# Performance work log

Hardware: AMD Instinct MI355X
Metric: run time of the kernel (lower is better)

Reference implementation:

```python
import jax, jax.numpy as jnp
import numpy as np
import math

N_NODES = 50000
N_EDGES = 640000
IN_FEATS = 128
HEADS = 8
OUT_FEATS = 16
D_FF = 4 * IN_FEATS


def setup_inputs() -> dict:
    key = jax.random.key(0)
    ks = jax.random.split(key, 10)
    s = 0.05
    return {
        "feat": jax.random.normal(ks[0], (N_NODES, IN_FEATS), jnp.float32),
        "src": jax.random.randint(ks[1], (N_EDGES,), 0, N_NODES, jnp.int32),
        "dst": jax.random.randint(ks[2], (N_EDGES,), 0, N_NODES, jnp.int32),
        "Wq": jax.random.normal(ks[3], (IN_FEATS, HEADS * OUT_FEATS), jnp.float32) * s,
        "Wk": jax.random.normal(ks[4], (IN_FEATS, HEADS * OUT_FEATS), jnp.float32) * s,
        "Wv": jax.random.normal(ks[5], (IN_FEATS, HEADS * OUT_FEATS), jnp.float32) * s,
        "ln1_g": jnp.ones((IN_FEATS,), jnp.float32),
        "ln1_b": jnp.zeros((IN_FEATS,), jnp.float32),
        "W1": jax.random.normal(ks[6], (IN_FEATS, D_FF), jnp.float32) * s,
        "b1": jnp.zeros((D_FF,), jnp.float32),
        "prelu_a": jnp.full((D_FF,), 0.25, jnp.float32),  # torch PReLU default init
        "W2": jax.random.normal(ks[7], (D_FF, IN_FEATS), jnp.float32) * s,
        "b2": jnp.zeros((IN_FEATS,), jnp.float32),
    }


def layer_norm(x, g, b, eps=1e-5):
    mu = jnp.mean(x, axis=-1, keepdims=True)
    var = jnp.mean(jnp.square(x - mu), axis=-1, keepdims=True)
    return (x - mu) * jax.lax.rsqrt(var + eps) * g + b


def reference(feat, src, dst, Wq, Wk, Wv, ln1_g, ln1_b, W1, b1, prelu_a, W2, b2):
    N = feat.shape[0]
    feat_c = jax.lax.stop_gradient(feat)  # feat.clone().detach()
    q = (feat @ Wq).reshape(N, HEADS, OUT_FEATS)
    k = (feat_c @ Wk).reshape(N, HEADS, OUT_FEATS)
    v = (feat_c @ Wv).reshape(N, HEADS, OUT_FEATS)

    # edge score: dot(k[src], q[dst]) per head -> [E, H]
    e = jnp.einsum('ehd,ehd->eh', k[src], q[dst]) / math.sqrt(OUT_FEATS * HEADS)

    # segment softmax over incoming edges of each dst node
    m = jax.ops.segment_max(e, dst, num_segments=N)          # [N, H]
    e_exp = jnp.exp(e - m[dst])                              # [E, H]
    denom = jax.ops.segment_sum(e_exp, dst, num_segments=N)  # [N, H]
    a = e_exp / denom[dst]                                   # [E, H]

    # weighted scatter-sum aggregation
    msg = v[src] * a[:, :, None]                             # [E, H, D]
    ft2 = jax.ops.segment_sum(msg, dst, num_segments=N)      # [N, H, D]

    rst = ft2.reshape(feat.shape) + feat
    # NOTE: original applies ln1 twice (ln2 is unused) -- reproduced faithfully
    rst = layer_norm(rst, ln1_g, ln1_b)
    h = rst @ W1 + b1
    h = jnp.where(h >= 0, h, prelu_a * h)                    # PReLU, per-channel
    ffn = h @ W2 + b2
    rst = layer_norm(rst + ffn, ln1_g, ln1_b)
    return rst
```

## Files before the change

kernel.cpp:

```cpp
#include <hip/hip_runtime.h>

#define N_NODES 50000
#define N_EDGES 640000
#define F 128
#define DFF 512
#define NB 196

using u32 = unsigned int;
using u16 = unsigned short;

typedef __bf16 bf16x8 __attribute__((ext_vector_type(8)));
typedef float f32x4 __attribute__((ext_vector_type(4)));

__device__ __forceinline__ float bf2f(u16 u) {
    return __uint_as_float(((u32)u) << 16);
}
__device__ __forceinline__ float blo(u32 p) { return __uint_as_float(p << 16); }
__device__ __forceinline__ float bhi(u32 p) { return __uint_as_float(p & 0xffff0000u); }
__device__ __forceinline__ u16 f2bf(float f) {
    u32 u = __float_as_uint(f);
    u += 0x7fffu + ((u >> 16) & 1u);
    return (u16)(u >> 16);
}
__device__ __forceinline__ u32 pack2(float a, float b) {
    return (u32)f2bf(a) | ((u32)f2bf(b) << 16);
}

__global__ void k_hist(const int* __restrict__ dst, int* __restrict__ cnt) {
    int e = blockIdx.x * 256 + threadIdx.x;
    if (e < N_EDGES) atomicAdd(&cnt[dst[e]], 1);
}

__global__ void k_bsum(const int* __restrict__ counts, int* __restrict__ bsum) {
    int i = blockIdx.x * 256 + threadIdx.x;
    int v = (i < N_NODES) ? counts[i] : 0;
#pragma unroll
    for (int off = 32; off >= 1; off >>= 1) v += __shfl_xor(v, off, 64);
    __shared__ int ws[4];
    int lane = threadIdx.x & 63, wid = threadIdx.x >> 6;
    if (lane == 0) ws[wid] = v;
    __syncthreads();
    if (threadIdx.x == 0) bsum[blockIdx.x] = ws[0] + ws[1] + ws[2] + ws[3];
}

__global__ void k_bscan(const int* __restrict__ bsum, int* __restrict__ boff) {
    int t = threadIdx.x;
    int v = (t < NB) ? bsum[t] : 0;
    int lane = t & 63, wid = t >> 6;
    int incl = v;
#pragma unroll
    for (int off = 1; off < 64; off <<= 1) {
        int u = __shfl_up(incl, off, 64);
        if (lane >= off) incl += u;
    }
    __shared__ int ws[4];
    if (lane == 63) ws[wid] = incl;
    __syncthreads();
    int wo = 0;
#pragma unroll
    for (int j = 0; j < 4; ++j) if (j < wid) wo += ws[j];
    if (t < NB) boff[t] = wo + incl - v;
}

__global__ void k_bfill(const int* __restrict__ counts, const int* __restrict__ boff,
                        int* __restrict__ row_ptr) {
    int b = blockIdx.x, t = threadIdx.x;
    int i = b * 256 + t;
    int v = (i < N_NODES) ? counts[i] : 0;
    int lane = t & 63, wid = t >> 6;
    int incl = v;
#pragma unroll
    for (int off = 1; off < 64; off <<= 1) {
        int u = __shfl_up(incl, off, 64);
        if (lane >= off) incl += u;
    }
    __shared__ int ws[4];
    if (lane == 63) ws[wid] = incl;
    __syncthreads();
    int wo = 0;
#pragma unroll
    for (int j = 0; j < 4; ++j) if (j < wid) wo += ws[j];
    if (i < N_NODES) row_ptr[i] = boff[b] + wo + incl - v;
    if (i == 0) row_ptr[N_NODES] = N_EDGES;
}

__global__ void k_fill(const int* __restrict__ src, const int* __restrict__ dst,
                       const int* __restrict__ row_ptr, int* __restrict__ fill,
                       int* __restrict__ csr_src) {
    int e = blockIdx.x * 256 + threadIdx.x;
    if (e < N_EDGES) {
        int d = dst[e];
        int pos = row_ptr[d] + atomicAdd(&fill[d], 1);
        csr_src[pos] = src[e];
    }
}

#define FEAT_UNITS (N_NODES * F / 4)
__global__ void k_prep(const float* __restrict__ feat, u16* __restrict__ featb,
                       const float* __restrict__ Wq, const float* __restrict__ Wk,
                       const float* __restrict__ Wv, const float* __restrict__ W1,
                       const float* __restrict__ W2, u16* __restrict__ WT) {
    int idx = blockIdx.x * 256 + threadIdx.x;
    if (idx < FEAT_UNITS) {
        float4 v = reinterpret_cast<const float4*>(feat)[idx];
        uint2 p;
        p.x = pack2(v.x, v.y);
        p.y = pack2(v.z, v.w);
        reinterpret_cast<uint2*>(featb)[idx] = p;
        return;
    }
    int wi = idx - FEAT_UNITS;
    if (wi >= 180224) return;
    if (wi < 49152) {
        int mi = wi >> 14;
        int local = wi & 16383;
        const float* W = (mi == 0) ? Wq : ((mi == 1) ? Wk : Wv);
        int n = local >> 7, k = local & 127;
        WT[wi] = f2bf(W[(size_t)k * 128 + n]);
    } else if (wi < 114688) {
        int local = wi - 49152;
        int n = local >> 7, k = local & 127;
        WT[wi] = f2bf(W1[(size_t)k * 512 + n]);
    } else {
        int local = wi - 114688;
        int n = local >> 9, k = local & 511;
        WT[wi] = f2bf(W2[(size_t)k * 128 + n]);
    }
}

template <int EPI>
__global__ __launch_bounds__(256) void k_mm(
    const u16* __restrict__ A, int lda,
    const u16* __restrict__ BT,
    void* __restrict__ Cv, int ldc,
    int K,
    const float* __restrict__ bias,
    const float* __restrict__ prelu,
    const u16* __restrict__ resid,
    const float* __restrict__ g,
    const float* __restrict__ bb)
{
    __shared__ u16 smem[17408];
    u16* sA = smem;
    u16* sB = smem + 128 * 64;
    u16* sC = smem;

    const int t = threadIdx.x;
    const int w = t >> 6;
    const int lane = t & 63;
    const int ln = lane & 15, q4 = lane >> 4;
    const int row0 = blockIdx.x * 128;
    const int cb = blockIdx.y * 128;

    f32x4 acc[2][8];
#pragma unroll
    for (int mt = 0; mt < 2; ++mt)
#pragma unroll
        for (int nt = 0; nt < 8; ++nt)
            acc[mt][nt] = (f32x4){0.f, 0.f, 0.f, 0.f};

    uint4 pa[4], pb[4];
#define LOAD_A(kc)                                                             \
    {                                                                          \
        _Pragma("unroll") for (int i = 0; i < 4; ++i) {                        \
            int u = i * 256 + t, r = u >> 3, k8 = (u & 7) * 8;                 \
            int row = row0 + r;                                                \
            uint4 val = make_uint4(0, 0, 0, 0);                                \
            if (row < N_NODES)                                                 \
                val = *reinterpret_cast<const uint4*>(A + (size_t)row * lda + (kc) + k8); \
            pa[i] = val;                                                       \
        }                                                                      \
    }
#define LOAD_B(kc)                                                             \
    {                                                                          \
        _Pragma("unroll") for (int i = 0; i < 4; ++i) {                        \
            int u = i * 256 + t, r = u >> 3, k8 = (u & 7) * 8;                 \
            pb[i] = *reinterpret_cast<const uint4*>(BT + (size_t)(cb + r) * K + (kc) + k8); \
        }                                                                      \
    }

    LOAD_A(0);
    LOAD_B(0);

    for (int kc = 0; kc < K; kc += 64) {
#pragma unroll
        for (int i = 0; i < 4; ++i) {
            int u = i * 256 + t, r = u >> 3, gi = u & 7;
            int off = (r * 8 + (gi ^ (r & 7))) * 8;
            *reinterpret_cast<uint4*>(&sA[off]) = pa[i];
            *reinterpret_cast<uint4*>(&sB[off]) = pb[i];
        }
        __syncthreads();
        if (kc + 64 < K) {
            LOAD_A(kc + 64);
            LOAD_B(kc + 64);
        }
#pragma unroll
        for (int ks = 0; ks < 2; ++ks) {
            const int gsw = ks * 4 + q4;
            const int rA0 = w * 32 + ln;
            const int rA1 = rA0 + 16;
            bf16x8 a0 = *reinterpret_cast<const bf16x8*>(&sA[(rA0 * 8 + (gsw ^ (rA0 & 7))) * 8]);
            bf16x8 a1 = *reinterpret_cast<const bf16x8*>(&sA[(rA1 * 8 + (gsw ^ (rA1 & 7))) * 8]);
#pragma unroll
            for (int nt = 0; nt < 8; ++nt) {
                const int rB = nt * 16 + ln;
                bf16x8 b = *reinterpret_cast<const bf16x8*>(&sB[(rB * 8 + (gsw ^ (rB & 7))) * 8]);
                acc[0][nt] = __builtin_amdgcn_mfma_f32_16x16x32_bf16(a0, b, acc[0][nt], 0, 0, 0);
                acc[1][nt] = __builtin_amdgcn_mfma_f32_16x16x32_bf16(a1, b, acc[1][nt], 0, 0, 0);
            }
        }
        __syncthreads();
    }
#undef LOAD_A
#undef LOAD_B

    if (EPI == 0 || EPI == 1) {
        float bs[8], pr[8];
        if (EPI == 1) {
#pragma unroll
            for (int nt = 0; nt < 8; ++nt) {
                int col = cb + nt * 16 + ln;
                bs[nt] = bias[col];
                pr[nt] = prelu[col];
            }
        }
#pragma unroll
        for (int mt = 0; mt < 2; ++mt)
#pragma unroll
            for (int nt = 0; nt < 8; ++nt)
#pragma unroll
                for (int j = 0; j < 4; ++j) {
                    float x = acc[mt][nt][j];
                    if (EPI == 1) {
                        x += bs[nt];
                        x = (x >= 0.f) ? x : pr[nt] * x;
                    }
                    sC[(w * 32 + mt * 16 + q4 * 4 + j) * 136 + nt * 16 + ln] = f2bf(x);
                }
        __syncthreads();
        if (EPI == 0 && cb != 0) {
            u32* C32 = (u32*)Cv;
            const u32 vflag = (cb == 256) ? 1u : 0u;
#pragma unroll
            for (int i = 0; i < 8; ++i) {
                int u = i * 256 + t;
                int r = u >> 4, c8 = (u & 15) * 8;
                int row = row0 + r;
                if (row < N_NODES) {
                    const u32* srow = reinterpret_cast<const u32*>(&sC[r * 136 + c8]);
                    u32 dw = (u32)row * 192u + 64u + (u32)c8 + vflag;
                    C32[dw]     = srow[0];
                    C32[dw + 2] = srow[1];
                    C32[dw + 4] = srow[2];
                    C32[dw + 6] = srow[3];
                }
            }
        } else {
            u16* C = (u16*)Cv;
#pragma unroll
            for (int i = 0; i < 8; ++i) {
                int u = i * 256 + t;
                int r = u >> 4, c8 = (u & 15) * 8;
                int row = row0 + r;
                if (row < N_NODES) {
                    uint4 val = *reinterpret_cast<const uint4*>(&sC[r * 136 + c8]);
                    *reinterpret_cast<uint4*>(&C[(size_t)row * ldc + cb + c8]) = val;
                }
            }
        }
    } else {
        float* C = (float*)Cv;
        float bs[8], gv[8], bv[8];
#pragma unroll
        for (int nt = 0; nt < 8; ++nt) {
            int col = nt * 16 + ln;
            bs[nt] = bias[col];
            gv[nt] = g[col];
            bv[nt] = bb[col];
        }
#pragma unroll
        for (int mt = 0; mt < 2; ++mt)
#pragma unroll
            for (int j = 0; j < 4; ++j) {
                int row = row0 + w * 32 + mt * 16 + q4 * 4 + j;
                bool ok = row < N_NODES;
                float vals[8];
                float s = 0.f, ss = 0.f;
#pragma unroll
                for (int nt = 0; nt < 8; ++nt) {
                    float x = acc[mt][nt][j] + bs[nt];
                    if (ok) x += bf2f(resid[(size_t)row * 128 + nt * 16 + ln]);
                    vals[nt] = x;
                    s += x; ss += x * x;
                }
                s += __shfl_xor(s, 8, 16); ss += __shfl_xor(ss, 8, 16);
                s += __shfl_xor(s, 4, 16); ss += __shfl_xor(ss, 4, 16);
                s += __shfl_xor(s, 2, 16); ss += __shfl_xor(ss, 2, 16);
                s += __shfl_xor(s, 1, 16); ss += __shfl_xor(ss, 1, 16);
                float mu = s * (1.f / 128.f);
                float var = ss * (1.f / 128.f) - mu * mu;
                float rs = rsqrtf(var + 1e-5f);
                if (ok) {
#pragma unroll
                    for (int nt = 0; nt < 8; ++nt)
                        C[(size_t)row * 128 + nt * 16 + ln] =
                            (vals[nt] - mu) * rs * gv[nt] + bv[nt];
                }
            }
    }
}

__global__ __launch_bounds__(256) void k_attn(
    const u32* __restrict__ Q32, const float* __restrict__ feat,
    const int* __restrict__ row_ptr, const int* __restrict__ csr_src,
    const float* __restrict__ g, const float* __restrict__ bb,
    u16* __restrict__ rstb)
{
    const int w = threadIdx.x >> 6;
    const int lane = threadIdx.x & 63;
    const int n = blockIdx.x * 4 + w;
    if (n >= N_NODES) return;
    const float scale = 0.08838834764831845f;

    const u32 qp = Q32[(u32)n * 192u + (u32)lane];
    const float q0 = blo(qp), q1 = bhi(qp);
    const int e0 = row_ptr[n], e1 = row_ptr[n + 1];
    const u32 kvlane = 64u + 2u * (u32)lane;

    float l = 0.f, a0 = 0.f, a1 = 0.f;

#define LD4(S, KV)                                                                      \
    {                                                                                   \
        KV[0] = *reinterpret_cast<const uint2*>(Q32 + (u32)(S).x * 192u + kvlane);      \
        KV[1] = *reinterpret_cast<const uint2*>(Q32 + (u32)(S).y * 192u + kvlane);      \
        KV[2] = *reinterpret_cast<const uint2*>(Q32 + (u32)(S).z * 192u + kvlane);      \
        KV[3] = *reinterpret_cast<const uint2*>(Q32 + (u32)(S).w * 192u + kvlane);      \
    }
#define CG(KV)                                                                          \
    {                                                                                   \
        float p0 = blo(KV[0].x) * q0 + bhi(KV[0].x) * q1;                               \
        float p1 = blo(KV[1].x) * q0 + bhi(KV[1].x) * q1;                               \
        float p2 = blo(KV[2].x) * q0 + bhi(KV[2].x) * q1;                               \
        float p3 = blo(KV[3].x) * q0 + bhi(KV[3].x) * q1;                               \
        p0 += __shfl_xor(p0, 4, 8); p1 += __shfl_xor(p1, 4, 8);                         \
        p2 += __shfl_xor(p2, 4, 8); p3 += __shfl_xor(p3, 4, 8);                         \
        p0 += __shfl_xor(p0, 2, 8); p1 += __shfl_xor(p1, 2, 8);                         \
        p2 += __shfl_xor(p2, 2, 8); p3 += __shfl_xor(p3, 2, 8);                         \
        p0 += __shfl_xor(p0, 1, 8); p1 += __shfl_xor(p1, 1, 8);                         \
        p2 += __shfl_xor(p2, 1, 8); p3 += __shfl_xor(p3, 1, 8);                         \
        float ea = __expf(p0 * scale), eb = __expf(p1 * scale);                         \
        float ec = __expf(p2 * scale), ed = __expf(p3 * scale);                         \
        l += (ea + eb) + (ec + ed);                                                     \
        a0 += ea * blo(KV[0].y) + eb * blo(KV[1].y) + ec * blo(KV[2].y) + ed * blo(KV[3].y); \
        a1 += ea * bhi(KV[0].y) + eb * bhi(KV[1].y) + ec * bhi(KV[2].y) + ed * bhi(KV[3].y); \
    }

    const int rem = e1 - e0;
    const int ng = rem >> 2;
    {
        int4 sA, sB, sCc;
        uint2 kvA[4], kvB[4], kvC[4];
        if (ng >= 1) { sA = *reinterpret_cast<const int4*>(csr_src + e0);      LD4(sA, kvA); }
        if (ng >= 2) { sB = *reinterpret_cast<const int4*>(csr_src + e0 + 4);  LD4(sB, kvB); }
        if (ng >= 3) { sCc = *reinterpret_cast<const int4*>(csr_src + e0 + 8); LD4(sCc, kvC); }
        int gq = 0;
        while (gq + 6 <= ng) {
            CG(kvA); sA = *reinterpret_cast<const int4*>(csr_src + e0 + (gq + 3) * 4); LD4(sA, kvA);
            CG(kvB); sB = *reinterpret_cast<const int4*>(csr_src + e0 + (gq + 4) * 4); LD4(sB, kvB);
            CG(kvC); sCc = *reinterpret_cast<const int4*>(csr_src + e0 + (gq + 5) * 4); LD4(sCc, kvC);
            gq += 3;
        }
        const int r = ng - gq;
        if (r == 1) { CG(kvA); }
        else if (r == 2) { CG(kvA); CG(kvB); }
        else if (r == 3) { CG(kvA); CG(kvB); CG(kvC); }
        else if (r == 4) {
            CG(kvA); sA = *reinterpret_cast<const int4*>(csr_src + e0 + (gq + 3) * 4); LD4(sA, kvA);
            CG(kvB); CG(kvC); CG(kvA);
        } else if (r == 5) {
            CG(kvA); sA = *reinterpret_cast<const int4*>(csr_src + e0 + (gq + 3) * 4); LD4(sA, kvA);
            CG(kvB); sB = *reinterpret_cast<const int4*>(csr_src + e0 + (gq + 4) * 4); LD4(sB, kvB);
            CG(kvC); CG(kvA); CG(kvB);
        }
    }
    for (int e = e0 + ng * 4; e < e1; ++e) {
        int s0 = csr_src[e];
        uint2 kv = *reinterpret_cast<const uint2*>(Q32 + (u32)s0 * 192u + kvlane);
        float p0 = blo(kv.x) * q0 + bhi(kv.x) * q1;
        p0 += __shfl_xor(p0, 4, 8);
        p0 += __shfl_xor(p0, 2, 8);
        p0 += __shfl_xor(p0, 1, 8);
        float ea = __expf(p0 * scale);
        l += ea;
        a0 += ea * blo(kv.y);
        a1 += ea * bhi(kv.y);
    }
#undef LD4
#undef CG

    float inv = (l > 0.f) ? 1.f / l : 0.f;
    const int c2 = lane * 2;
    const float2 fr = *reinterpret_cast<const float2*>(feat + (size_t)n * 128 + c2);
    float x0 = a0 * inv + fr.x;
    float x1 = a1 * inv + fr.y;

    float sum = x0 + x1, sq = x0 * x0 + x1 * x1;
#pragma unroll
    for (int off = 32; off >= 1; off >>= 1) {
        sum += __shfl_xor(sum, off, 64);
        sq += __shfl_xor(sq, off, 64);
    }
    float mu = sum * (1.f / 128.f);
    float var = sq * (1.f / 128.f) - mu * mu;
    float rs = rsqrtf(var + 1e-5f);
    float y0 = (x0 - mu) * rs * g[c2] + bb[c2];
    float y1 = (x1 - mu) * rs * g[c2 + 1] + bb[c2 + 1];
    reinterpret_cast<u32*>(rstb)[(size_t)n * 64 + lane] = pack2(y0, y1);
}

extern "C" void kernel_launch(void* const* d_in, const int* in_sizes, int n_in,
                              void* d_out, int out_size, void* d_ws, size_t ws_size,
                              hipStream_t stream)
{
    const float* feat = (const float*)d_in[0];
    const int* src    = (const int*)d_in[1];
    const int* dst    = (const int*)d_in[2];
    const float* Wq   = (const float*)d_in[3];
    const float* Wk   = (const float*)d_in[4];
    const float* Wv   = (const float*)d_in[5];
    const float* ln_g = (const float*)d_in[6];
    const float* ln_b = (const float*)d_in[7];
    const float* W1   = (const float*)d_in[8];
    const float* b1   = (const float*)d_in[9];
    const float* pa   = (const float*)d_in[10];
    const float* W2   = (const float*)d_in[11];
    const float* b2   = (const float*)d_in[12];

    u16* qkv   = (u16*)d_ws;
    u16* h     = qkv + (size_t)N_NODES * 384;
    u16* featb = h;
    u16* rstb  = h + (size_t)N_NODES * 512;
    u16* WT    = rstb + (size_t)N_NODES * 128;
    u16* BqkvT = WT;
    u16* W1T   = WT + 49152;
    u16* W2T   = WT + 114688;
    int* counts  = (int*)(WT + 180224);
    int* fill    = counts + N_NODES;
    int* row_ptr = fill + N_NODES;
    int* csr_src = row_ptr + N_NODES + 1;
    int* bsum    = csr_src + N_EDGES;
    int* boff    = bsum + NB;

    k_prep<<<(FEAT_UNITS + 180224 + 255) / 256, 256, 0, stream>>>(
        feat, featb, Wq, Wk, Wv, W1, W2, WT);

    hipMemsetAsync(counts, 0, sizeof(int) * 2 * N_NODES, stream);
    k_hist<<<(N_EDGES + 255) / 256, 256, 0, stream>>>(dst, counts);
    k_bsum<<<NB, 256, 0, stream>>>(counts, bsum);
    k_bscan<<<1, 256, 0, stream>>>(bsum, boff);
    k_bfill<<<NB, 256, 0, stream>>>(counts, boff, row_ptr);
    k_fill<<<(N_EDGES + 255) / 256, 256, 0, stream>>>(src, dst, row_ptr, fill, csr_src);

    const int MBK = (N_NODES + 127) / 128;

    dim3 gqkv(MBK, 3);
    k_mm<0><<<gqkv, 256, 0, stream>>>(featb, 128, BqkvT, qkv, 384, 128,
                                      nullptr, nullptr, nullptr, nullptr, nullptr);

    k_attn<<<(N_NODES + 3) / 4, 256, 0, stream>>>((const u32*)qkv, feat, row_ptr, csr_src,
                                                  ln_g, ln_b, rstb);

    dim3 gf1(MBK, 4);
    k_mm<1><<<gf1, 256, 0, stream>>>(rstb, 128, W1T, h, 512, 128,
                                     b1, pa, nullptr, nullptr, nullptr);

    dim3 gf2(MBK, 1);
    k_mm<2><<<gf2, 256, 0, stream>>>(h, 512, W2T, d_out, 128, 512,
                                     b2, nullptr, rstb, ln_g, ln_b);
}
```

Measured before the change: 350.9 us.

## Fuse histogram into prep, merge block scan into fill, simplify attention prefetch

```diff
diff --git a/kernel.cpp b/kernel.cpp
--- a/kernel.cpp
+++ b/kernel.cpp
@@ -26,8 +26,42 @@
     return (u32)f2bf(a) | ((u32)f2bf(b) << 16);
 }
 
-__global__ void k_hist(const int* __restrict__ dst, int* __restrict__ cnt) {
-    int e = blockIdx.x * 256 + threadIdx.x;
+#define FEAT_UNITS (N_NODES * F / 4)
+#define PH_TOTAL (FEAT_UNITS + 180224 + N_EDGES)
+__global__ void k_prep(const float* __restrict__ feat, u16* __restrict__ featb,
+                       const float* __restrict__ Wq, const float* __restrict__ Wk,
+                       const float* __restrict__ Wv, const float* __restrict__ W1,
+                       const float* __restrict__ W2, u16* __restrict__ WT,
+                       const int* __restrict__ dst, int* __restrict__ cnt) {
+    int idx = blockIdx.x * 256 + threadIdx.x;
+    if (idx < FEAT_UNITS) {
+        float4 v = reinterpret_cast<const float4*>(feat)[idx];
+        uint2 p;
+        p.x = pack2(v.x, v.y);
+        p.y = pack2(v.z, v.w);
+        reinterpret_cast<uint2*>(featb)[idx] = p;
+        return;
+    }
+    int wi = idx - FEAT_UNITS;
+    if (wi < 180224) {
+        if (wi < 49152) {
+            int mi = wi >> 14;
+            int local = wi & 16383;
+            const float* W = (mi == 0) ? Wq : ((mi == 1) ? Wk : Wv);
+            int n = local >> 7, k = local & 127;
+            WT[wi] = f2bf(W[(size_t)k * 128 + n]);
+        } else if (wi < 114688) {
+            int local = wi - 49152;
+            int n = local >> 7, k = local & 127;
+            WT[wi] = f2bf(W1[(size_t)k * 512 + n]);
+        } else {
+            int local = wi - 114688;
+            int n = local >> 9, k = local & 511;
+            WT[wi] = f2bf(W2[(size_t)k * 128 + n]);
+        }
+        return;
+    }
+    int e = wi - 180224;
     if (e < N_EDGES) atomicAdd(&cnt[dst[e]], 1);
 }
 
@@ -43,44 +77,43 @@
     if (threadIdx.x == 0) bsum[blockIdx.x] = ws[0] + ws[1] + ws[2] + ws[3];
 }
 
-__global__ void k_bscan(const int* __restrict__ bsum, int* __restrict__ boff) {
-    int t = threadIdx.x;
-    int v = (t < NB) ? bsum[t] : 0;
+__global__ void k_bfill(const int* __restrict__ counts, const int* __restrict__ bsum,
+                        int* __restrict__ row_ptr) {
+    int b = blockIdx.x, t = threadIdx.x;
     int lane = t & 63, wid = t >> 6;
+    __shared__ int ws[4];
+    __shared__ int sboff[256];
+
+    int bv = (t < NB) ? bsum[t] : 0;
+    int bincl = bv;
+#pragma unroll
+    for (int off = 1; off < 64; off <<= 1) {
+        int u = __shfl_up(bincl, off, 64);
+        if (lane >= off) bincl += u;
+    }
+    if (lane == 63) ws[wid] = bincl;
+    __syncthreads();
+    int bwo = 0;
+#pragma unroll
+    for (int j = 0; j < 4; ++j) if (j < wid) bwo += ws[j];
+    sboff[t] = bwo + bincl - bv;
+    __syncthreads();
+    const int boff = sboff[b];
+
+    int i = b * 256 + t;
+    int v = (i < N_NODES) ? counts[i] : 0;
     int incl = v;
 #pragma unroll
     for (int off = 1; off < 64; off <<= 1) {
         int u = __shfl_up(incl, off, 64);
         if (lane >= off) incl += u;
     }
-    __shared__ int ws[4];
     if (lane == 63) ws[wid] = incl;
     __syncthreads();
     int wo = 0;
 #pragma unroll
     for (int j = 0; j < 4; ++j) if (j < wid) wo += ws[j];
-    if (t < NB) boff[t] = wo + incl - v;
-}
-
-__global__ void k_bfill(const int* __restrict__ counts, const int* __restrict__ boff,
-                        int* __restrict__ row_ptr) {
-    int b = blockIdx.x, t = threadIdx.x;
-    int i = b * 256 + t;
-    int v = (i < N_NODES) ? counts[i] : 0;
-    int lane = t & 63, wid = t >> 6;
-    int incl = v;
-#pragma unroll
-    for (int off = 1; off < 64; off <<= 1) {
-        int u = __shfl_up(incl, off, 64);
-        if (lane >= off) incl += u;
-    }
-    __shared__ int ws[4];
-    if (lane == 63) ws[wid] = incl;
-    __syncthreads();
-    int wo = 0;
-#pragma unroll
-    for (int j = 0; j < 4; ++j) if (j < wid) wo += ws[j];
-    if (i < N_NODES) row_ptr[i] = boff[b] + wo + incl - v;
+    if (i < N_NODES) row_ptr[i] = boff + wo + incl - v;
     if (i == 0) row_ptr[N_NODES] = N_EDGES;
 }
 
@@ -92,39 +125,6 @@
         int d = dst[e];
         int pos = row_ptr[d] + atomicAdd(&fill[d], 1);
         csr_src[pos] = src[e];
-    }
-}
-
-#define FEAT_UNITS (N_NODES * F / 4)
-__global__ void k_prep(const float* __restrict__ feat, u16* __restrict__ featb,
-                       const float* __restrict__ Wq, const float* __restrict__ Wk,
-                       const float* __restrict__ Wv, const float* __restrict__ W1,
-                       const float* __restrict__ W2, u16* __restrict__ WT) {
-    int idx = blockIdx.x * 256 + threadIdx.x;
-    if (idx < FEAT_UNITS) {
-        float4 v = reinterpret_cast<const float4*>(feat)[idx];
-        uint2 p;
-        p.x = pack2(v.x, v.y);
-        p.y = pack2(v.z, v.w);
-        reinterpret_cast<uint2*>(featb)[idx] = p;
-        return;
-    }
-    int wi = idx - FEAT_UNITS;
-    if (wi >= 180224) return;
-    if (wi < 49152) {
-        int mi = wi >> 14;
-        int local = wi & 16383;
-        const float* W = (mi == 0) ? Wq : ((mi == 1) ? Wk : Wv);
-        int n = local >> 7, k = local & 127;
-        WT[wi] = f2bf(W[(size_t)k * 128 + n]);
-    } else if (wi < 114688) {
-        int local = wi - 49152;
-        int n = local >> 7, k = local & 127;
-        WT[wi] = f2bf(W1[(size_t)k * 512 + n]);
-    } else {
-        int local = wi - 114688;
-        int n = local >> 9, k = local & 511;
-        WT[wi] = f2bf(W2[(size_t)k * 128 + n]);
     }
 }
 
@@ -356,35 +356,35 @@
         a1 += ea * bhi(KV[0].y) + eb * bhi(KV[1].y) + ec * bhi(KV[2].y) + ed * bhi(KV[3].y); \
     }
 
-    const int rem = e1 - e0;
-    const int ng = rem >> 2;
+    int e = e0;
+    int rem = e1 - e0;
     {
-        int4 sA, sB, sCc;
-        uint2 kvA[4], kvB[4], kvC[4];
-        if (ng >= 1) { sA = *reinterpret_cast<const int4*>(csr_src + e0);      LD4(sA, kvA); }
-        if (ng >= 2) { sB = *reinterpret_cast<const int4*>(csr_src + e0 + 4);  LD4(sB, kvB); }
-        if (ng >= 3) { sCc = *reinterpret_cast<const int4*>(csr_src + e0 + 8); LD4(sCc, kvC); }
-        int gq = 0;
-        while (gq + 6 <= ng) {
-            CG(kvA); sA = *reinterpret_cast<const int4*>(csr_src + e0 + (gq + 3) * 4); LD4(sA, kvA);
-            CG(kvB); sB = *reinterpret_cast<const int4*>(csr_src + e0 + (gq + 4) * 4); LD4(sB, kvB);
-            CG(kvC); sCc = *reinterpret_cast<const int4*>(csr_src + e0 + (gq + 5) * 4); LD4(sCc, kvC);
-            gq += 3;
-        }
-        const int r = ng - gq;
-        if (r == 1) { CG(kvA); }
-        else if (r == 2) { CG(kvA); CG(kvB); }
-        else if (r == 3) { CG(kvA); CG(kvB); CG(kvC); }
-        else if (r == 4) {
-            CG(kvA); sA = *reinterpret_cast<const int4*>(csr_src + e0 + (gq + 3) * 4); LD4(sA, kvA);
-            CG(kvB); CG(kvC); CG(kvA);
-        } else if (r == 5) {
-            CG(kvA); sA = *reinterpret_cast<const int4*>(csr_src + e0 + (gq + 3) * 4); LD4(sA, kvA);
-            CG(kvB); sB = *reinterpret_cast<const int4*>(csr_src + e0 + (gq + 4) * 4); LD4(sB, kvB);
-            CG(kvC); CG(kvA); CG(kvB);
-        }
-    }
-    for (int e = e0 + ng * 4; e < e1; ++e) {
+        int4 sA, sB;
+        uint2 kvA[4], kvB[4];
+        if (rem >= 4) {
+            sA = *reinterpret_cast<const int4*>(csr_src + e);
+            LD4(sA, kvA);
+            if (rem >= 8) {
+                sB = *reinterpret_cast<const int4*>(csr_src + e + 4);
+                while (true) {
+                    if (rem >= 12) sA = *reinterpret_cast<const int4*>(csr_src + e + 8);
+                    LD4(sB, kvB);
+                    CG(kvA);
+                    e += 4; rem -= 4;
+                    if (rem < 8) { CG(kvB); e += 4; rem -= 4; break; }
+                    if (rem >= 12) sB = *reinterpret_cast<const int4*>(csr_src + e + 8);
+                    LD4(sA, kvA);
+                    CG(kvB);
+                    e += 4; rem -= 4;
+                    if (rem < 8) { CG(kvA); e += 4; rem -= 4; break; }
+                }
+            } else {
+                CG(kvA);
+                e += 4; rem -= 4;
+            }
+        }
+    }
+    for (; e < e1; ++e) {
         int s0 = csr_src[e];
         uint2 kv = *reinterpret_cast<const uint2*>(Q32 + (u32)s0 * 192u + kvlane);
         float p0 = blo(kv.x) * q0 + bhi(kv.x) * q1;
@@ -450,16 +450,13 @@
     int* row_ptr = fill + N_NODES;
     int* csr_src = row_ptr + N_NODES + 1;
     int* bsum    = csr_src + N_EDGES;
-    int* boff    = bsum + NB;
-
-    k_prep<<<(FEAT_UNITS + 180224 + 255) / 256, 256, 0, stream>>>(
-        feat, featb, Wq, Wk, Wv, W1, W2, WT);
 
     hipMemsetAsync(counts, 0, sizeof(int) * 2 * N_NODES, stream);
-    k_hist<<<(N_EDGES + 255) / 256, 256, 0, stream>>>(dst, counts);
+    k_prep<<<(PH_TOTAL + 255) / 256, 256, 0, stream>>>(
+        feat, featb, Wq, Wk, Wv, W1, W2, WT, dst, counts);
+
     k_bsum<<<NB, 256, 0, stream>>>(counts, bsum);
-    k_bscan<<<1, 256, 0, stream>>>(bsum, boff);
-    k_bfill<<<NB, 256, 0, stream>>>(counts, boff, row_ptr);
+    k_bfill<<<NB, 256, 0, stream>>>(counts, bsum, row_ptr);
     k_fill<<<(N_EDGES + 255) / 256, 256, 0, stream>>>(src, dst, row_ptr, fill, csr_src);
 
     const int MBK = (N_NODES + 127) / 128;
```

New measurement: 324.4 us. 7.6% less time.
